# Optimization experiments

Hardware: AMD Instinct MI355X
Metric: run time of the kernel (lower is better)

## Reference

```python
import jax, jax.numpy as jnp
import numpy as np

N_NODES = 100000
N_EDGES = 3200000
NFEAT, NHID, NCLASS = 512, 256, 64


def spmm(edge_src, edge_dst, edge_weight, dense):
    # out[dst] += w * dense[src]  -- sparse adjacency @ dense
    msgs = dense[edge_src] * edge_weight[:, None]  # [E, d]
    return jax.ops.segment_sum(msgs, edge_dst, num_segments=N_NODES)


def setup_inputs() -> dict:
    key = jax.random.key(0)
    ks = jax.random.split(key, 8)
    x = jax.random.normal(ks[0], (N_NODES, NFEAT), dtype=jnp.float32)
    edge_src = jax.random.randint(ks[1], (N_EDGES,), 0, N_NODES, dtype=jnp.int32)
    edge_dst = jax.random.randint(ks[2], (N_EDGES,), 0, N_NODES, dtype=jnp.int32)
    edge_weight = jax.random.uniform(ks[3], (N_EDGES,), dtype=jnp.float32)
    W1 = jax.random.normal(ks[4], (NFEAT, NHID), dtype=jnp.float32) / np.sqrt(NFEAT)
    b1 = jax.random.normal(ks[5], (NHID,), dtype=jnp.float32) * 0.01
    W2 = jax.random.normal(ks[6], (NHID, NCLASS), dtype=jnp.float32) / np.sqrt(NHID)
    b2 = jax.random.normal(ks[7], (NCLASS,), dtype=jnp.float32) * 0.01
    return {"x": x, "edge_src": edge_src, "edge_dst": edge_dst,
            "edge_weight": edge_weight, "W1": W1, "b1": b1, "W2": W2, "b2": b2}


def reference(x, edge_src, edge_dst, edge_weight, W1, b1, W2, b2):
    # Layer 1: GraphConvolution -> relu -> dropout(identity, eval mode)
    support0 = x @ W1                                   # [N, nhid]
    Z0 = spmm(edge_src, edge_dst, edge_weight, support0) + b1
    H0 = jax.nn.relu(Z0)
    # F.dropout with training=False is identity
    # Layer 2: GraphConvolution -> log_softmax
    support1 = H0 @ W2                                  # [N, nclass]
    Z1 = spmm(edge_src, edge_dst, edge_weight, support1) + b2
    H1 = jax.nn.log_softmax(Z1, axis=1)
    return H1
```

## Files before the change

### kernel.cpp

```cpp
#include <hip/hip_runtime.h>
#include <hip/hip_bf16.h>

static constexpr int N_NODES = 100000;
static constexpr int N_EDGES = 3200000;
static constexpr int NFEAT   = 512;
static constexpr int NHID    = 256;
static constexpr int NCLASS  = 64;

static constexpr int BK2_SHIFT = 8;
static constexpr int NBUCK2 = (N_NODES + 255) >> 8;
static constexpr int BIN_EPB = 8192;
static constexpr int NBIN = (N_EDGES + BIN_EPB - 1) / BIN_EPB;

using short8 = __attribute__((ext_vector_type(8))) short;
using f32x4  = __attribute__((ext_vector_type(4))) float;
using fv4    = __attribute__((ext_vector_type(4))) float;
using fv2    = __attribute__((ext_vector_type(2))) float;
using iv4    = __attribute__((ext_vector_type(4))) int;
using iv2    = __attribute__((ext_vector_type(2))) int;
using fvec4  = __attribute__((ext_vector_type(4))) float;

__device__ __forceinline__ short f2bf_bits(float f) {
    __hip_bfloat16 h = __float2bfloat16(f);
    return *reinterpret_cast<short*>(&h);
}

__device__ __forceinline__ unsigned char f2fp8(float v) {
    int p = __builtin_amdgcn_cvt_pk_fp8_f32(v, v, 0, false);
    return (unsigned char)(p & 0xff);
}

__device__ __forceinline__ void fp8x8_acc_pk(int vx, int vy, float w, fv2* acc2) {
    fv2 w2; w2[0] = w; w2[1] = w;
    acc2[0] += w2 * __builtin_amdgcn_cvt_pk_f32_fp8(vx, false);
    acc2[1] += w2 * __builtin_amdgcn_cvt_pk_f32_fp8(vx, true);
    acc2[2] += w2 * __builtin_amdgcn_cvt_pk_f32_fp8(vy, false);
    acc2[3] += w2 * __builtin_amdgcn_cvt_pk_f32_fp8(vy, true);
}

__device__ __forceinline__ void fp8x16_acc_pk(iv4 v, float w, fv2* acc2) {
    fp8x8_acc_pk(v.x, v.y, w, acc2);
    fp8x8_acc_pk(v.z, v.w, w, acc2 + 4);
}

#define GLOBAL_TO_LDS(gsrc, ldst)                                                        \
    __builtin_amdgcn_global_load_lds((const __attribute__((address_space(1))) void*)(gsrc), \
                                     (__attribute__((address_space(3))) void*)(ldst), 16, 0, 0)

__global__ __launch_bounds__(1024) void bucket_hist_kernel(const int* __restrict__ edst,
                                                           int* __restrict__ bcnt) {
    __shared__ int lcount[NBUCK2];
    int tid = threadIdx.x;
    if (tid < NBUCK2) lcount[tid] = 0;
    __syncthreads();
    int e0 = blockIdx.x * BIN_EPB + tid * 8;
    if (e0 < N_EDGES) {
        iv4 d0 = __builtin_nontemporal_load((const iv4*)(edst + e0));
        iv4 d1 = __builtin_nontemporal_load((const iv4*)(edst + e0 + 4));
        atomicAdd(&lcount[d0.x >> BK2_SHIFT], 1);
        atomicAdd(&lcount[d0.y >> BK2_SHIFT], 1);
        atomicAdd(&lcount[d0.z >> BK2_SHIFT], 1);
        atomicAdd(&lcount[d0.w >> BK2_SHIFT], 1);
        atomicAdd(&lcount[d1.x >> BK2_SHIFT], 1);
        atomicAdd(&lcount[d1.y >> BK2_SHIFT], 1);
        atomicAdd(&lcount[d1.z >> BK2_SHIFT], 1);
        atomicAdd(&lcount[d1.w >> BK2_SHIFT], 1);
    }
    __syncthreads();
    if (tid < NBUCK2) atomicAdd(&bcnt[tid], lcount[tid]);
}

__global__ __launch_bounds__(512) void bucket_scan_kernel(const int* __restrict__ bcnt,
                                                          int* __restrict__ boffs,
                                                          int* __restrict__ bucket_cursor,
                                                          int* __restrict__ row_ptr) {
    __shared__ int sd[512];
    int t = threadIdx.x;
    int v = (t < NBUCK2) ? bcnt[t] : 0;
    sd[t] = v;
    __syncthreads();
    for (int off = 1; off < 512; off <<= 1) {
        int x = (t >= off) ? sd[t - off] : 0;
        __syncthreads();
        sd[t] += x;
        __syncthreads();
    }
    int excl = sd[t] - v;
    if (t < NBUCK2) { boffs[t] = excl; bucket_cursor[t] = excl; }
    if (t == 0) { boffs[NBUCK2] = N_EDGES; row_ptr[N_NODES] = N_EDGES; }
}

__global__ __launch_bounds__(1024) void bin_kernel(const int* __restrict__ esrc,
                                                   const int* __restrict__ edst,
                                                   const float* __restrict__ ew,
                                                   int* __restrict__ bucket_cursor,
                                                   int2* __restrict__ spk) {
    __shared__ int lcount[NBUCK2];
    __shared__ int lbase[NBUCK2];
    int tid = threadIdx.x;
    if (tid < NBUCK2) lcount[tid] = 0;
    __syncthreads();
    int e0 = blockIdx.x * BIN_EPB + tid * 8;
    bool act = (e0 < N_EDGES);
    int dd[8], ss[8], wb[8], bi[8], rank[8];
    if (act) {
        iv4 d0 = __builtin_nontemporal_load((const iv4*)(edst + e0));
        iv4 d1 = __builtin_nontemporal_load((const iv4*)(edst + e0 + 4));
        iv4 s0 = __builtin_nontemporal_load((const iv4*)(esrc + e0));
        iv4 s1 = __builtin_nontemporal_load((const iv4*)(esrc + e0 + 4));
        iv4 w0 = __builtin_nontemporal_load((const iv4*)(ew + e0));
        iv4 w1 = __builtin_nontemporal_load((const iv4*)(ew + e0 + 4));
        dd[0]=d0.x; dd[1]=d0.y; dd[2]=d0.z; dd[3]=d0.w;
        dd[4]=d1.x; dd[5]=d1.y; dd[6]=d1.z; dd[7]=d1.w;
        ss[0]=s0.x; ss[1]=s0.y; ss[2]=s0.z; ss[3]=s0.w;
        ss[4]=s1.x; ss[5]=s1.y; ss[6]=s1.z; ss[7]=s1.w;
        wb[0]=w0.x; wb[1]=w0.y; wb[2]=w0.z; wb[3]=w0.w;
        wb[4]=w1.x; wb[5]=w1.y; wb[6]=w1.z; wb[7]=w1.w;
#pragma unroll
        for (int k = 0; k < 8; ++k) {
            bi[k] = dd[k] >> BK2_SHIFT;
            rank[k] = atomicAdd(&lcount[bi[k]], 1);
        }
    }
    __syncthreads();
    if (tid < NBUCK2) lbase[tid] = atomicAdd(&bucket_cursor[tid], lcount[tid]);
    __syncthreads();
    if (act) {
#pragma unroll
        for (int k = 0; k < 8; ++k) {
            int pos = lbase[bi[k]] + rank[k];
            int ld = dd[k] & 255;
            spk[pos] = make_int2(ss[k] | (ld << 17), wb[k]);
        }
    }
}

__global__ __launch_bounds__(512) void finalize_bucket_kernel(const int2* __restrict__ spk,
                                                              const int* __restrict__ boffs,
                                                              int* __restrict__ row_ptr,
                                                              int2* __restrict__ pk) {
    int b = blockIdx.x;
    int nb0 = b << BK2_SHIFT;
    int nnode = N_NODES - nb0; if (nnode > 256) nnode = 256;
    int start = boffs[b], end = boffs[b + 1];
    __shared__ int cnt[256];
    __shared__ int pref[256];
    int tid = threadIdx.x;
    if (tid < 256) cnt[tid] = 0;
    __syncthreads();
    for (int e = start + tid; e < end; e += 512) {
        int ld = ((unsigned)spk[e].x >> 17) & 255;
        atomicAdd(&cnt[ld], 1);
    }
    __syncthreads();
    if (tid < 256) pref[tid] = cnt[tid];
    __syncthreads();
    for (int off = 1; off < 256; off <<= 1) {
        int x = 0;
        if (tid < 256 && tid >= off) x = pref[tid - off];
        __syncthreads();
        if (tid < 256) pref[tid] += x;
        __syncthreads();
    }
    if (tid < 256) {
        int excl = pref[tid] - cnt[tid];
        if (tid < nnode) row_ptr[nb0 + tid] = start + excl;
        cnt[tid] = excl;
    }
    __syncthreads();
    for (int e = start + tid; e < end; e += 512) {
        int2 s = spk[e];
        int ld = ((unsigned)s.x >> 17) & 255;
        int pos = start + atomicAdd(&cnt[ld], 1);
        pk[pos] = make_int2(s.x & 0x1FFFF, s.y);
    }
}

__global__ __launch_bounds__(256) void transpose_w_kernel(const float* __restrict__ W,
                                                          __hip_bfloat16* __restrict__ WT,
                                                          int K, int N) {
    int idx = blockIdx.x * 256 + threadIdx.x;
    if (idx < K * N) {
        int k = idx / N, n = idx % N;
        WT[(size_t)n * K + k] = __float2bfloat16(W[idx]);
    }
}

__global__ __launch_bounds__(512) void gemm1_mfma(const float* __restrict__ A,
                                                  const __hip_bfloat16* __restrict__ BT,
                                                  unsigned char* __restrict__ C8,
                                                  int M) {
    constexpr int K = NFEAT;
    constexpr int N = NHID;
    constexpr int BM = 128, BK = 32;
    constexpr int NSTEP = K / BK;
    __shared__ __align__(16) float          As[2][BM * BK];
    __shared__ __align__(16) __hip_bfloat16 Bs[2][256 * BK];
    const int tid = threadIdx.x;
    const int lane = tid & 63, wave = tid >> 6;
    const int wr = wave >> 2, wc = wave & 3;
    const int laneRow = lane & 15, laneK = lane >> 4;
    const int row0 = blockIdx.x * BM;

    f32x4 acc[4][4] = {};

    auto STAGE = [&](int step) {
        {
            float* dst = As[step & 1];
#pragma unroll
            for (int it = 0; it < 2; ++it) {
                int q = wave * 2 + it;
                int r = q * 8 + (lane >> 3);
                int c16 = lane & 7;
                int src_c = (c16 ^ ((r & 3) << 1)) * 4;
                int rg = row0 + r; rg = (rg < M) ? rg : (M - 1);
                const float* src = A + (size_t)rg * K + step * BK + src_c;
                GLOBAL_TO_LDS(src, dst + q * 256 + lane * 4);
            }
        }
        {
            __hip_bfloat16* dst = Bs[step & 1];
#pragma unroll
            for (int it = 0; it < 2; ++it) {
                int idx2 = tid + it * 512;
                int n = idx2 >> 2;
                int gk = (idx2 & 3) ^ ((n >> 1) & 3);
                const __hip_bfloat16* src = BT + (size_t)n * K + step * BK + gk * 8;
                GLOBAL_TO_LDS(src, dst + (size_t)idx2 * 8);
            }
        }
    };

    STAGE(0);

#pragma unroll
    for (int t = 0; t < NSTEP; ++t) {
        __syncthreads();
        if (t + 1 < NSTEP) STAGE(t + 1);
        short8 af[4];
#pragma unroll
        for (int i = 0; i < 4; ++i) {
            int rr = wr * 64 + i * 16 + laneRow;
            int ck = laneK ^ (rr & 3);
            const float* ap = As[t & 1] + rr * BK + ck * 8;
            fv4 a0 = *(const fv4*)ap;
            fv4 a1 = *(const fv4*)(ap + 4);
            short8 v;
#pragma unroll
            for (int j = 0; j < 4; ++j) v[j] = f2bf_bits(a0[j]);
#pragma unroll
            for (int j = 0; j < 4; ++j) v[4 + j] = f2bf_bits(a1[j]);
            af[i] = v;
        }
        short8 bfr[4];
#pragma unroll
        for (int j = 0; j < 4; ++j) {
            int n = wc * 64 + j * 16 + laneRow;
            int pg = laneK ^ ((n >> 1) & 3);
            bfr[j] = *(const short8*)(Bs[t & 1] + n * BK + pg * 8);
        }
#pragma unroll
        for (int i = 0; i < 4; ++i)
#pragma unroll
            for (int j = 0; j < 4; ++j)
                acc[i][j] = __builtin_amdgcn_mfma_f32_16x16x32_bf16(af[i], bfr[j], acc[i][j], 0, 0, 0);
    }
#pragma unroll
    for (int i = 0; i < 4; ++i) {
        int rbase = row0 + wr * 64 + i * 16 + laneK * 4;
#pragma unroll
        for (int j = 0; j < 4; ++j) {
            int col = wc * 64 + j * 16 + laneRow;
#pragma unroll
            for (int q = 0; q < 4; ++q) {
                int row = rbase + q;
                if (row < M) C8[(size_t)row * N + col] = f2fp8(acc[i][j][q]);
            }
        }
    }
}

__global__ __launch_bounds__(256) void gemm2_mfma(const __hip_bfloat16* __restrict__ A,
                                                  const __hip_bfloat16* __restrict__ BT,
                                                  unsigned char* __restrict__ C8,
                                                  int M) {
    constexpr int K = NHID;
    constexpr int N = NCLASS;
    constexpr int BM = 128;
    __shared__ __align__(16) __hip_bfloat16 Bs[N * K];
    const int tid = threadIdx.x;
    const int lane = tid & 63, wave = tid >> 6;
    const int wr = wave >> 1, wc = wave & 1;
    const int laneRow = lane & 15, laneK = lane >> 4;
    const int row0 = blockIdx.x * BM;

#pragma unroll
    for (int it = 0; it < 8; ++it) {
        int idx = tid + it * 256;
        int n = idx >> 5;
        int kk = (idx & 31) ^ (n & 7);
        const __hip_bfloat16* src = BT + (size_t)n * K + kk * 8;
        GLOBAL_TO_LDS(src, Bs + (size_t)idx * 8);
    }

    int arow[4];
#pragma unroll
    for (int i = 0; i < 4; ++i) {
        int r = row0 + wr * 64 + i * 16 + laneRow;
        arow[i] = (r < M) ? r : (M - 1);
    }

    f32x4 acc[4][2] = {};
    __syncthreads();

#pragma unroll
    for (int k0 = 0; k0 < K; k0 += 32) {
        short8 af[4];
#pragma unroll
        for (int i = 0; i < 4; ++i)
            af[i] = *(const short8*)(A + (size_t)arow[i] * K + k0 + laneK * 8);
        short8 bfr[2];
#pragma unroll
        for (int j = 0; j < 2; ++j) {
            int n = wc * 32 + j * 16 + laneRow;
            int kkw = (k0 >> 3) + laneK;
            int pkk = kkw ^ (n & 7);
            bfr[j] = *(const short8*)(Bs + (size_t)n * 32 * 8 + pkk * 8);
        }
#pragma unroll
        for (int i = 0; i < 4; ++i)
#pragma unroll
            for (int j = 0; j < 2; ++j)
                acc[i][j] = __builtin_amdgcn_mfma_f32_16x16x32_bf16(af[i], bfr[j], acc[i][j], 0, 0, 0);
    }

#pragma unroll
    for (int i = 0; i < 4; ++i) {
        int rbase = row0 + wr * 64 + i * 16 + laneK * 4;
#pragma unroll
        for (int j = 0; j < 2; ++j) {
            int col = wc * 32 + j * 16 + laneRow;
#pragma unroll
            for (int q = 0; q < 4; ++q) {
                int row = rbase + q;
                if (row < M) C8[(size_t)row * N + col] = f2fp8(acc[i][j][q]);
            }
        }
    }
}

__global__ __launch_bounds__(256) void spmm1_kernel(const unsigned char* __restrict__ s0_8,
                                                    const int* __restrict__ row_ptr,
                                                    const int2* __restrict__ pk,
                                                    const float* __restrict__ b1,
                                                    __hip_bfloat16* __restrict__ H0) {
    int node = blockIdx.x * 4 + (threadIdx.x >> 6);
    int lane = threadIdx.x & 63;
    int j = lane >> 4;
    int c = lane & 15;
    int coff = c * 16;
    int beg = row_ptr[node], end = row_ptr[node + 1];
    fv2 acc2[8] = {};
    for (int base = beg; base + j < end; base += 8) {
        int2 pe0 = pk[base + j];
        int i1 = base + 4 + j;
        int2 pe1 = (i1 < end) ? pk[i1] : make_int2(0, 0);
        float w0 = __int_as_float(pe0.y);
        float w1 = __int_as_float(pe1.y);
        iv4 v0 = *(const iv4*)(s0_8 + (size_t)pe0.x * NHID + coff);
        iv4 v1 = *(const iv4*)(s0_8 + (size_t)pe1.x * NHID + coff);
        fp8x16_acc_pk(v0, w0, acc2);
        fp8x16_acc_pk(v1, w1, acc2);
    }
    float accf[16];
#pragma unroll
    for (int k = 0; k < 8; ++k) { accf[2 * k] = acc2[k][0]; accf[2 * k + 1] = acc2[k][1]; }
#pragma unroll
    for (int m = 16; m < 64; m <<= 1)
#pragma unroll
        for (int k = 0; k < 16; ++k) accf[k] += __shfl_xor(accf[k], m);
    if (lane < 16) {
        short8 o0, o1;
#pragma unroll
        for (int k = 0; k < 8; ++k)  o0[k] = f2bf_bits(fmaxf(accf[k] + b1[coff + k], 0.f));
#pragma unroll
        for (int k = 0; k < 8; ++k)  o1[k] = f2bf_bits(fmaxf(accf[8 + k] + b1[coff + 8 + k], 0.f));
        __hip_bfloat16* dst = H0 + (size_t)node * NHID + coff;
        *(short8*)dst = o0;
        *(short8*)(dst + 8) = o1;
    }
}

__global__ __launch_bounds__(256) void spmm2_softmax_kernel(const unsigned char* __restrict__ s1_8,
                                                            const int* __restrict__ row_ptr,
                                                            const int2* __restrict__ pk,
                                                            const float* __restrict__ b2,
                                                            float* __restrict__ out) {
    int node = blockIdx.x * 4 + (threadIdx.x >> 6);
    int lane = threadIdx.x & 63;
    int j = lane >> 3;
    int c = lane & 7;
    int beg = row_ptr[node], end = row_ptr[node + 1];
    fv2 acc2[4] = {};
    for (int base = beg; base + j < end; base += 16) {
        int2 pe0 = pk[base + j];
        int i1 = base + 8 + j;
        int2 pe1 = (i1 < end) ? pk[i1] : make_int2(0, 0);
        float w0 = __int_as_float(pe0.y);
        float w1 = __int_as_float(pe1.y);
        int2 v0 = *(const int2*)(s1_8 + (size_t)pe0.x * NCLASS + c * 8);
        int2 v1 = *(const int2*)(s1_8 + (size_t)pe1.x * NCLASS + c * 8);
        fp8x8_acc_pk(v0.x, v0.y, w0, acc2);
        fp8x8_acc_pk(v1.x, v1.y, w1, acc2);
    }
    float acc[8];
#pragma unroll
    for (int k = 0; k < 4; ++k) { acc[2 * k] = acc2[k][0]; acc[2 * k + 1] = acc2[k][1]; }
#pragma unroll
    for (int m = 8; m < 64; m <<= 1)
#pragma unroll
        for (int k = 0; k < 8; ++k) acc[k] += __shfl_xor(acc[k], m);

    fv4 blo = *(const fv4*)(b2 + c * 8);
    fv4 bhi = *(const fv4*)(b2 + c * 8 + 4);
    float z[8];
#pragma unroll
    for (int k = 0; k < 4; ++k) z[k] = acc[k] + blo[k];
#pragma unroll
    for (int k = 0; k < 4; ++k) z[4 + k] = acc[4 + k] + bhi[k];

    float mx = z[0];
#pragma unroll
    for (int k = 1; k < 8; ++k) mx = fmaxf(mx, z[k]);
#pragma unroll
    for (int m = 1; m < 8; m <<= 1) mx = fmaxf(mx, __shfl_xor(mx, m));
    float s = 0.f;
#pragma unroll
    for (int k = 0; k < 8; ++k) s += __expf(z[k] - mx);
#pragma unroll
    for (int m = 1; m < 8; m <<= 1) s += __shfl_xor(s, m);
    float lg = __logf(s);
    if (lane < 8) {
        f32x4 o0, o1;
#pragma unroll
        for (int k = 0; k < 4; ++k) o0[k] = z[k] - mx - lg;
#pragma unroll
        for (int k = 0; k < 4; ++k) o1[k] = z[4 + k] - mx - lg;
        float* dst = out + (size_t)node * NCLASS + c * 8;
        *(f32x4*)dst = o0;
        *(f32x4*)(dst + 4) = o1;
    }
}

extern "C" void kernel_launch(void* const* d_in, const int* in_sizes, int n_in,
                              void* d_out, int out_size, void* d_ws, size_t ws_size,
                              hipStream_t stream) {
    const float* x    = (const float*)d_in[0];
    const int*   esrc = (const int*)d_in[1];
    const int*   edst = (const int*)d_in[2];
    const float* ew   = (const float*)d_in[3];
    const float* W1   = (const float*)d_in[4];
    const float* b1   = (const float*)d_in[5];
    const float* W2   = (const float*)d_in[6];
    const float* b2   = (const float*)d_in[7];
    float* out = (float*)d_out;

    char* ws = (char*)d_ws;
    size_t off = 0;
    auto alloc = [&](size_t bytes) {
        size_t o = off;
        off = (off + bytes + 255) & ~(size_t)255;
        return o;
    };
    unsigned char* support0 = (unsigned char*)(ws + alloc((size_t)N_NODES * NHID));
    __hip_bfloat16* H0      = (__hip_bfloat16*)(ws + alloc((size_t)N_NODES * NHID * 2));
    unsigned char* support1 = (unsigned char*)(ws + alloc((size_t)N_NODES * NCLASS));
    int2*  pk         = (int2*)(ws + alloc((size_t)N_EDGES * 8));
    int2*  spk        = (int2*)(ws + alloc((size_t)N_EDGES * 8));
    int*   row_ptr    = (int*)(ws + alloc((size_t)(N_NODES + 1) * 4));
    int*   bcnt       = (int*)(ws + alloc(512 * 4));
    int*   boffs      = (int*)(ws + alloc(512 * 4));
    int*   bucket_cursor = (int*)(ws + alloc(512 * 4));
    __hip_bfloat16* W1T = (__hip_bfloat16*)(ws + alloc((size_t)NHID * NFEAT * 2));
    __hip_bfloat16* W2T = (__hip_bfloat16*)(ws + alloc((size_t)NCLASS * NHID * 2));

    transpose_w_kernel<<<(NFEAT * NHID + 255) / 256, 256, 0, stream>>>(W1, W1T, NFEAT, NHID);
    transpose_w_kernel<<<(NHID * NCLASS + 255) / 256, 256, 0, stream>>>(W2, W2T, NHID, NCLASS);

    hipMemsetAsync(bcnt, 0, 512 * 4, stream);
    bucket_hist_kernel<<<NBIN, 1024, 0, stream>>>(edst, bcnt);
    bucket_scan_kernel<<<1, 512, 0, stream>>>(bcnt, boffs, bucket_cursor, row_ptr);
    bin_kernel<<<NBIN, 1024, 0, stream>>>(esrc, edst, ew, bucket_cursor, spk);
    finalize_bucket_kernel<<<NBUCK2, 512, 0, stream>>>(spk, boffs, row_ptr, pk);

    gemm1_mfma<<<(N_NODES + 127) / 128, 512, 0, stream>>>(x, W1T, support0, N_NODES);
    spmm1_kernel<<<N_NODES / 4, 256, 0, stream>>>(support0, row_ptr, pk, b1, H0);

    gemm2_mfma<<<(N_NODES + 127) / 128, 256, 0, stream>>>(H0, W2T, support1, N_NODES);
    spmm2_softmax_kernel<<<N_NODES / 4, 256, 0, stream>>>(support1, row_ptr, pk, b2, out);
}
```

Baseline: 334.0 us.

## Fuse layer-1 SpMM with second GEMM through LDS, dropping H0 buffer

Merges the layer-1 SpMM (bias+ReLU) and the H0@W2 GEMM into one kernel. Each block aggregates 16 nodes into a swizzled bf16 tile in LDS and multiplies it by W2 held in LDS with MFMA. This removes the global write and reread of the 100000x256 bf16 H0 array and one kernel launch. In exchange every block reloads the 32KB W2 into LDS, each wave now processes 4 nodes serially, and the larger LDS use may lower occupancy. The hipMemsetAsync for the bucket counters is also replaced by a tiny zeroing kernel.

```diff
diff --git a/kernel.cpp b/kernel.cpp
--- a/kernel.cpp
+++ b/kernel.cpp
@@ -46,6 +46,8 @@
 #define GLOBAL_TO_LDS(gsrc, ldst)                                                        \
     __builtin_amdgcn_global_load_lds((const __attribute__((address_space(1))) void*)(gsrc), \
                                      (__attribute__((address_space(3))) void*)(ldst), 16, 0, 0)
+
+__global__ void zero512_kernel(int* __restrict__ p) { p[threadIdx.x] = 0; }
 
 __global__ __launch_bounds__(1024) void bucket_hist_kernel(const int* __restrict__ edst,
                                                            int* __restrict__ bcnt) {
@@ -280,114 +282,84 @@
     }
 }
 
-__global__ __launch_bounds__(256) void gemm2_mfma(const __hip_bfloat16* __restrict__ A,
-                                                  const __hip_bfloat16* __restrict__ BT,
-                                                  unsigned char* __restrict__ C8,
-                                                  int M) {
-    constexpr int K = NHID;
-    constexpr int N = NCLASS;
-    constexpr int BM = 128;
-    __shared__ __align__(16) __hip_bfloat16 Bs[N * K];
+__global__ __launch_bounds__(256) void spmm1_gemm2_kernel(const unsigned char* __restrict__ s0_8,
+                                                          const int* __restrict__ row_ptr,
+                                                          const int2* __restrict__ pk,
+                                                          const float* __restrict__ b1,
+                                                          const __hip_bfloat16* __restrict__ W2T,
+                                                          unsigned char* __restrict__ S1) {
+    __shared__ __align__(16) __hip_bfloat16 H0s[16 * NHID];
+    __shared__ __align__(16) __hip_bfloat16 W2s[NCLASS * NHID];
     const int tid = threadIdx.x;
     const int lane = tid & 63, wave = tid >> 6;
-    const int wr = wave >> 1, wc = wave & 1;
     const int laneRow = lane & 15, laneK = lane >> 4;
-    const int row0 = blockIdx.x * BM;
+    const int nbase = blockIdx.x * 16;
 
 #pragma unroll
     for (int it = 0; it < 8; ++it) {
         int idx = tid + it * 256;
         int n = idx >> 5;
         int kk = (idx & 31) ^ (n & 7);
-        const __hip_bfloat16* src = BT + (size_t)n * K + kk * 8;
-        GLOBAL_TO_LDS(src, Bs + (size_t)idx * 8);
-    }
-
-    int arow[4];
-#pragma unroll
-    for (int i = 0; i < 4; ++i) {
-        int r = row0 + wr * 64 + i * 16 + laneRow;
-        arow[i] = (r < M) ? r : (M - 1);
-    }
-
-    f32x4 acc[4][2] = {};
-    __syncthreads();
-
-#pragma unroll
-    for (int k0 = 0; k0 < K; k0 += 32) {
-        short8 af[4];
-#pragma unroll
-        for (int i = 0; i < 4; ++i)
-            af[i] = *(const short8*)(A + (size_t)arow[i] * K + k0 + laneK * 8);
-        short8 bfr[2];
-#pragma unroll
-        for (int j = 0; j < 2; ++j) {
-            int n = wc * 32 + j * 16 + laneRow;
-            int kkw = (k0 >> 3) + laneK;
-            int pkk = kkw ^ (n & 7);
-            bfr[j] = *(const short8*)(Bs + (size_t)n * 32 * 8 + pkk * 8);
-        }
-#pragma unroll
-        for (int i = 0; i < 4; ++i)
-#pragma unroll
-            for (int j = 0; j < 2; ++j)
-                acc[i][j] = __builtin_amdgcn_mfma_f32_16x16x32_bf16(af[i], bfr[j], acc[i][j], 0, 0, 0);
-    }
-
-#pragma unroll
-    for (int i = 0; i < 4; ++i) {
-        int rbase = row0 + wr * 64 + i * 16 + laneK * 4;
-#pragma unroll
-        for (int j = 0; j < 2; ++j) {
-            int col = wc * 32 + j * 16 + laneRow;
-#pragma unroll
-            for (int q = 0; q < 4; ++q) {
-                int row = rbase + q;
-                if (row < M) C8[(size_t)row * N + col] = f2fp8(acc[i][j][q]);
-            }
-        }
-    }
-}
-
-__global__ __launch_bounds__(256) void spmm1_kernel(const unsigned char* __restrict__ s0_8,
-                                                    const int* __restrict__ row_ptr,
-                                                    const int2* __restrict__ pk,
-                                                    const float* __restrict__ b1,
-                                                    __hip_bfloat16* __restrict__ H0) {
-    int node = blockIdx.x * 4 + (threadIdx.x >> 6);
-    int lane = threadIdx.x & 63;
+        const __hip_bfloat16* src = W2T + (size_t)n * NHID + kk * 8;
+        GLOBAL_TO_LDS(src, W2s + (size_t)idx * 8);
+    }
+
     int j = lane >> 4;
-    int c = lane & 15;
+    int c = laneRow;
     int coff = c * 16;
-    int beg = row_ptr[node], end = row_ptr[node + 1];
-    fv2 acc2[8] = {};
-    for (int base = beg; base + j < end; base += 8) {
-        int2 pe0 = pk[base + j];
-        int i1 = base + 4 + j;
-        int2 pe1 = (i1 < end) ? pk[i1] : make_int2(0, 0);
-        float w0 = __int_as_float(pe0.y);
-        float w1 = __int_as_float(pe1.y);
-        iv4 v0 = *(const iv4*)(s0_8 + (size_t)pe0.x * NHID + coff);
-        iv4 v1 = *(const iv4*)(s0_8 + (size_t)pe1.x * NHID + coff);
-        fp8x16_acc_pk(v0, w0, acc2);
-        fp8x16_acc_pk(v1, w1, acc2);
-    }
-    float accf[16];
-#pragma unroll
-    for (int k = 0; k < 8; ++k) { accf[2 * k] = acc2[k][0]; accf[2 * k + 1] = acc2[k][1]; }
-#pragma unroll
-    for (int m = 16; m < 64; m <<= 1)
-#pragma unroll
-        for (int k = 0; k < 16; ++k) accf[k] += __shfl_xor(accf[k], m);
-    if (lane < 16) {
-        short8 o0, o1;
-#pragma unroll
-        for (int k = 0; k < 8; ++k)  o0[k] = f2bf_bits(fmaxf(accf[k] + b1[coff + k], 0.f));
-#pragma unroll
-        for (int k = 0; k < 8; ++k)  o1[k] = f2bf_bits(fmaxf(accf[8 + k] + b1[coff + 8 + k], 0.f));
-        __hip_bfloat16* dst = H0 + (size_t)node * NHID + coff;
-        *(short8*)dst = o0;
-        *(short8*)(dst + 8) = o1;
+#pragma unroll
+    for (int ln4 = 0; ln4 < 4; ++ln4) {
+        int r = wave * 4 + ln4;
+        int node = nbase + r;
+        int beg = row_ptr[node], end = row_ptr[node + 1];
+        fv2 acc2[8] = {};
+        for (int base = beg; base + j < end; base += 8) {
+            int2 pe0 = pk[base + j];
+            int i1 = base + 4 + j;
+            int2 pe1 = (i1 < end) ? pk[i1] : make_int2(0, 0);
+            float w0 = __int_as_float(pe0.y);
+            float w1 = __int_as_float(pe1.y);
+            iv4 v0 = *(const iv4*)(s0_8 + (size_t)pe0.x * NHID + coff);
+            iv4 v1 = *(const iv4*)(s0_8 + (size_t)pe1.x * NHID + coff);
+            fp8x16_acc_pk(v0, w0, acc2);
+            fp8x16_acc_pk(v1, w1, acc2);
+        }
+        float accf[16];
+#pragma unroll
+        for (int k = 0; k < 8; ++k) { accf[2 * k] = acc2[k][0]; accf[2 * k + 1] = acc2[k][1]; }
+#pragma unroll
+        for (int m = 16; m < 64; m <<= 1)
+#pragma unroll
+            for (int k = 0; k < 16; ++k) accf[k] += __shfl_xor(accf[k], m);
+        if (lane < 16) {
+            short8 o0, o1;
+#pragma unroll
+            for (int k = 0; k < 8; ++k) o0[k] = f2bf_bits(fmaxf(accf[k] + b1[coff + k], 0.f));
+#pragma unroll
+            for (int k = 0; k < 8; ++k) o1[k] = f2bf_bits(fmaxf(accf[8 + k] + b1[coff + 8 + k], 0.f));
+            int p0 = (2 * c) ^ (r & 15);
+            int p1 = (2 * c + 1) ^ (r & 15);
+            *(short8*)(H0s + r * NHID + p0 * 8) = o0;
+            *(short8*)(H0s + r * NHID + p1 * 8) = o1;
+        }
+    }
+    __syncthreads();
+
+    f32x4 acc = {};
+#pragma unroll
+    for (int s = 0; s < 8; ++s) {
+        int ckA = (4 * s + laneK) ^ (laneRow & 15);
+        short8 af = *(const short8*)(H0s + laneRow * NHID + ckA * 8);
+        int n = wave * 16 + laneRow;
+        int pkk = (4 * s + laneK) ^ (n & 7);
+        short8 bf = *(const short8*)(W2s + n * NHID + pkk * 8);
+        acc = __builtin_amdgcn_mfma_f32_16x16x32_bf16(af, bf, acc, 0, 0, 0);
+    }
+    int col = wave * 16 + laneRow;
+#pragma unroll
+    for (int q = 0; q < 4; ++q) {
+        int row = laneK * 4 + q;
+        S1[(size_t)(nbase + row) * NCLASS + col] = f2fp8(acc[q]);
     }
 }
 
@@ -473,7 +445,6 @@
         return o;
     };
     unsigned char* support0 = (unsigned char*)(ws + alloc((size_t)N_NODES * NHID));
-    __hip_bfloat16* H0      = (__hip_bfloat16*)(ws + alloc((size_t)N_NODES * NHID * 2));
     unsigned char* support1 = (unsigned char*)(ws + alloc((size_t)N_NODES * NCLASS));
     int2*  pk         = (int2*)(ws + alloc((size_t)N_EDGES * 8));
     int2*  spk        = (int2*)(ws + alloc((size_t)N_EDGES * 8));
@@ -487,15 +458,16 @@
     transpose_w_kernel<<<(NFEAT * NHID + 255) / 256, 256, 0, stream>>>(W1, W1T, NFEAT, NHID);
     transpose_w_kernel<<<(NHID * NCLASS + 255) / 256, 256, 0, stream>>>(W2, W2T, NHID, NCLASS);
 
-    hipMemsetAsync(bcnt, 0, 512 * 4, stream);
+    zero512_kernel<<<1, 512, 0, stream>>>(bcnt);
     bucket_hist_kernel<<<NBIN, 1024, 0, stream>>>(edst, bcnt);
     bucket_scan_kernel<<<1, 512, 0, stream>>>(bcnt, boffs, bucket_cursor, row_ptr);
     bin_kernel<<<NBIN, 1024, 0, stream>>>(esrc, edst, ew, bucket_cursor, spk);
     finalize_bucket_kernel<<<NBUCK2, 512, 0, stream>>>(spk, boffs, row_ptr, pk);
 
     gemm1_mfma<<<(N_NODES + 127) / 128, 512, 0, stream>>>(x, W1T, support0, N_NODES);
-    spmm1_kernel<<<N_NODES / 4, 256, 0, stream>>>(support0, row_ptr, pk, b1, H0);
-
-    gemm2_mfma<<<(N_NODES + 127) / 128, 256, 0, stream>>>(H0, W2T, support1, N_NODES);
+
+    spmm1_gemm2_kernel<<<N_NODES / 16, 256, 0, stream>>>(support0, row_ptr, pk, b1, W2T,
+                                                         support1);
+
     spmm2_softmax_kernel<<<N_NODES / 4, 256, 0, stream>>>(support1, row_ptr, pk, b2, out);
 }
```

After: 349.4 us. 1.05x slower.
